# Kernel optimization log

Hardware: AMD Instinct MI355X
Metric: run time of the kernel (lower is better)

Reference implementation:

```python
import jax, jax.numpy as jnp
import numpy as np

N_NODES = 100000
N_EDGES = 3200000
EMBED = 64
DIMS = [(64, 32), (32, 16)]  # (in_dim, out_dim) per Aggregator layer
EPS = 1e-12


def setup_inputs() -> dict:
    key = jax.random.key(0)
    ks = jax.random.split(key, 16)
    inp = {
        "aux_info_all": jax.random.normal(ks[0], (N_NODES, 3), jnp.float32),
        "entity_embed": jax.random.normal(ks[1], (N_NODES, EMBED), jnp.float32) * 0.1,
        "aux_W": jax.random.normal(ks[2], (EMBED, 3), jnp.float32) * 0.3,
        "aux_b": jnp.zeros((EMBED,), jnp.float32),
        "edge_vals": jax.random.uniform(ks[3], (N_EDGES,), jnp.float32),
        "edge_rows": jax.random.randint(ks[4], (N_EDGES,), 0, N_NODES, jnp.int32),
        "edge_cols": jax.random.randint(ks[5], (N_EDGES,), 0, N_NODES, jnp.int32),
    }
    for li, (din, dout) in enumerate(DIMS):
        s = (2.0 / (din + dout)) ** 0.5  # xavier-ish scale
        inp[f"W1_{li}"] = jax.random.normal(ks[6 + 4 * li], (dout, din), jnp.float32) * s
        inp[f"b1_{li}"] = jnp.zeros((dout,), jnp.float32)
        inp[f"W2_{li}"] = jax.random.normal(ks[7 + 4 * li], (dout, din), jnp.float32) * s
        inp[f"b2_{li}"] = jnp.zeros((dout,), jnp.float32)
    return inp


def _l2norm(x):
    return x / jnp.maximum(jnp.linalg.norm(x, axis=1, keepdims=True), EPS)


def reference(aux_info_all, entity_embed, aux_W, aux_b,
              W1_0, b1_0, W2_0, b2_0, W1_1, b1_1, W2_1, b2_1,
              edge_vals, edge_rows, edge_cols):
    # holographic fusion: entity_embed * (1 + tanh(Linear(aux)))
    aux_vec = jnp.tanh(aux_info_all @ aux_W.T + aux_b)
    ego = entity_embed * (1.0 + aux_vec)  # [N, 64]
    all_embed = [ego]
    layers = [(W1_0, b1_0, W2_0, b2_0), (W1_1, b1_1, W2_1, b2_1)]
    for W1, b1, W2, b2 in layers:
        # sparse A_in @ ego: gather messages over edges, segment-sum by destination row
        msgs = edge_vals[:, None] * ego[edge_cols]  # [E, d]
        side = jax.ops.segment_sum(msgs, edge_rows, num_segments=N_NODES)  # [N, d]
        sum_e = jax.nn.leaky_relu((ego + side) @ W1.T + b1)  # bi-interaction branch 1
        bi_e = jax.nn.leaky_relu((ego * side) @ W2.T + b2)   # bi-interaction branch 2
        ego = sum_e + bi_e  # (dropout p=0 in eval)
        all_embed.append(_l2norm(ego))
    return jnp.concatenate(all_embed, axis=1)  # [N, 64+32+16]
```

## Files before the change

kernel.cpp:

```cpp
#include <hip/hip_runtime.h>
#include <math.h>

#define NN 100000
#define NE 3200000
#define OUTD 112
#define BROWS 512
#define NBUCK 196
#define FILL_CH 8192
#define FILL_B ((NE + FILL_CH - 1) / FILL_CH)
#define BLD1_T 1024
#define SORT_T 1024
#define FUSE_B ((NN * 64 + BLD1_T - 1) / BLD1_T)

__device__ inline unsigned short f32_to_bf16(float f) {
    unsigned u = __float_as_uint(f);
    u += 0x7FFFu + ((u >> 16) & 1u);
    return (unsigned short)(u >> 16);
}
__device__ inline float bf16_bits_to_f32(unsigned b) {
    return __uint_as_float(b << 16);
}

__global__ __launch_bounds__(BLD1_T) void prep_kernel(
    const int* __restrict__ rows,
    int* __restrict__ gcount,
    int* __restrict__ bhistT,
    const float* __restrict__ aux_info,
    const float* __restrict__ entity,
    const float* __restrict__ aux_W,
    const float* __restrict__ aux_b,
    unsigned short* __restrict__ ego0h,
    float* __restrict__ out)
{
    __shared__ int h[NBUCK];
    if (blockIdx.x < FILL_B) {
        for (int i = threadIdx.x; i < NBUCK; i += BLD1_T) h[i] = 0;
        __syncthreads();
        int base = blockIdx.x * FILL_CH;
        int nE = NE - base; if (nE > FILL_CH) nE = FILL_CH;
        for (int i = threadIdx.x; i < nE; i += BLD1_T)
            atomicAdd(&h[rows[base + i] >> 9], 1);
        __syncthreads();
        for (int i = threadIdx.x; i < NBUCK; i += BLD1_T) {
            int c = h[i];
            bhistT[i * FILL_B + blockIdx.x] = c;
            if (c) atomicAdd(&gcount[i], c);
        }
    } else {
        int idx = (blockIdx.x - FILL_B) * BLD1_T + threadIdx.x;
        if (idx >= NN * 64) return;
        int n = idx >> 6;
        int j = idx & 63;
        float a0 = aux_info[n * 3 + 0];
        float a1 = aux_info[n * 3 + 1];
        float a2 = aux_info[n * 3 + 2];
        float w0 = aux_W[j * 3 + 0];
        float w1 = aux_W[j * 3 + 1];
        float w2 = aux_W[j * 3 + 2];
        float t = tanhf(fmaf(a0, w0, fmaf(a1, w1, fmaf(a2, w2, aux_b[j]))));
        float e = entity[idx] * (1.0f + t);
        ego0h[idx] = f32_to_bf16(e);
        out[(size_t)n * OUTD + j] = e;
    }
}

__global__ void cursor_scan_kernel(const int* __restrict__ bhistT,
                                   const int* __restrict__ gcount,
                                   int* __restrict__ bucket_base,
                                   int* __restrict__ cursor) {
    static_assert(FILL_B <= 512, "scan width");
    __shared__ int sh[512];
    __shared__ int bb[256];
    int b = blockIdx.x;
    int t = threadIdx.x;
    int gv = (t < NBUCK) ? gcount[t] : 0;
    if (t < 256) bb[t] = gv;
    __syncthreads();
    for (int off = 1; off < 256; off <<= 1) {
        int u = (t >= off && t < 256) ? bb[t - off] : 0;
        __syncthreads();
        if (t < 256) bb[t] += u;
        __syncthreads();
    }
    int base_b = (b > 0) ? bb[b - 1] : 0;
    if (t == 0) bucket_base[b] = base_b;
    if (b == 0 && t == 0) bucket_base[NBUCK] = bb[NBUCK - 1];
    int v = (t < FILL_B) ? bhistT[b * FILL_B + t] : 0;
    sh[t] = v;
    __syncthreads();
    for (int off = 1; off < 512; off <<= 1) {
        int u = (t >= off) ? sh[t - off] : 0;
        __syncthreads();
        sh[t] += u;
        __syncthreads();
    }
    if (t < FILL_B) cursor[b * FILL_B + t] = base_b + sh[t] - v;
}

__global__ void bucket_fill_kernel(const int* __restrict__ rows,
                                   const int* __restrict__ cols,
                                   const float* __restrict__ vals,
                                   const int* __restrict__ cursor,
                                   int2* __restrict__ edges_b) {
    __shared__ int curs[NBUCK];
    int base = blockIdx.x * FILL_CH;
    int nE = NE - base; if (nE > FILL_CH) nE = FILL_CH;
    for (int i = threadIdx.x; i < NBUCK; i += BLD1_T)
        curs[i] = cursor[i * FILL_B + blockIdx.x];
    __syncthreads();
    for (int i = threadIdx.x; i < nE; i += BLD1_T) {
        int r = rows[base + i];
        int p = atomicAdd(&curs[r >> 9], 1);
        edges_b[p] = make_int2(cols[base + i] | ((r & (BROWS - 1)) << 17),
                               __float_as_int(vals[base + i]));
    }
}

__global__ __launch_bounds__(SORT_T) void csr_sort_kernel(
    const int2* __restrict__ edges_b,
    const int* __restrict__ bucket_base,
    unsigned int* __restrict__ edges,
    int* __restrict__ row_ptr) {
    __shared__ int cnt[BROWS];
    __shared__ int scn[BROWS];
    __shared__ int curs[BROWS];
    int b = blockIdx.x;
    int beg = bucket_base[b], end = bucket_base[b + 1];
    int t = threadIdx.x;
    if (t < BROWS) cnt[t] = 0;
    __syncthreads();
    for (int i = beg + t; i < end; i += SORT_T)
        atomicAdd(&cnt[(edges_b[i].x >> 17) & (BROWS - 1)], 1);
    __syncthreads();
    if (t < BROWS) scn[t] = cnt[t];
    __syncthreads();
    for (int off = 1; off < BROWS; off <<= 1) {
        int v = (t >= off && t < BROWS) ? scn[t - off] : 0;
        __syncthreads();
        if (t < BROWS) scn[t] += v;
        __syncthreads();
    }
    if (t < BROWS) {
        int excl = scn[t] - cnt[t];
        int n = b * BROWS + t;
        if (n <= NN) row_ptr[n] = beg + excl;
        curs[t] = beg + excl;
    }
    __syncthreads();
    for (int i = beg + t; i < end; i += SORT_T) {
        int2 e = edges_b[i];
        int rl = (e.x >> 17) & (BROWS - 1);
        int p = atomicAdd(&curs[rl], 1);
        unsigned int vb = f32_to_bf16(__int_as_float(e.y)) & 0x7FFFu;
        edges[p] = (unsigned int)(e.x & 0x1FFFF) | (vb << 17);
    }
}

template <int FO, int UU>
__device__ __forceinline__ void gacc(const uint4* __restrict__ egoh4,
                                     const unsigned int* __restrict__ edges,
                                     int i, int es, int fo, float a[8]) {
    constexpr int ES = 32 / FO;
    unsigned ew[UU];
    uint4 g[UU];
#pragma unroll
    for (int u = 0; u < UU; ++u) ew[u] = edges[i + u * ES + es];
#pragma unroll
    for (int u = 0; u < UU; ++u)
        g[u] = egoh4[(size_t)(ew[u] & 0x1FFFFu) * FO + fo];
#pragma unroll
    for (int u = 0; u < UU; ++u) {
        float v = __uint_as_float((ew[u] >> 1) & 0xFFFF0000u);
        a[0] = fmaf(v, __uint_as_float(g[u].x << 16), a[0]);
        a[1] = fmaf(v, __uint_as_float(g[u].x & 0xFFFF0000u), a[1]);
        a[2] = fmaf(v, __uint_as_float(g[u].y << 16), a[2]);
        a[3] = fmaf(v, __uint_as_float(g[u].y & 0xFFFF0000u), a[3]);
        a[4] = fmaf(v, __uint_as_float(g[u].z << 16), a[4]);
        a[5] = fmaf(v, __uint_as_float(g[u].z & 0xFFFF0000u), a[5]);
        a[6] = fmaf(v, __uint_as_float(g[u].w << 16), a[6]);
        a[7] = fmaf(v, __uint_as_float(g[u].w & 0xFFFF0000u), a[7]);
    }
}

template <int D>
__global__ __launch_bounds__(256) void gather_kernel(
    const uint4* __restrict__ egoh4,
    const unsigned int* __restrict__ edges,
    const int* __restrict__ row_ptr,
    float* __restrict__ side) {
    constexpr int FO = D / 8;
    constexpr int ES = 32 / FO;
    const int gt = blockIdx.x * 256 + threadIdx.x;
    const int n  = gt >> 5;
    const int li = gt & 31;
    const int es = li / FO;
    const int fo = li % FO;
    if (n >= NN) return;
    int beg = row_ptr[n];
    int end = row_ptr[n + 1];
    float a[8] = {0.f, 0.f, 0.f, 0.f, 0.f, 0.f, 0.f, 0.f};
    int i = beg;
    for (; i + 16 <= end; i += 16) gacc<FO, 16 / ES>(egoh4, edges, i, es, fo, a);
    for (; i + ES <= end; i += ES) gacc<FO, 1>(egoh4, edges, i, es, fo, a);
    if (i + es < end) {
        unsigned ew = edges[i + es];
        uint4 g = egoh4[(size_t)(ew & 0x1FFFFu) * FO + fo];
        float v = __uint_as_float((ew >> 1) & 0xFFFF0000u);
        a[0] = fmaf(v, __uint_as_float(g.x << 16), a[0]);
        a[1] = fmaf(v, __uint_as_float(g.x & 0xFFFF0000u), a[1]);
        a[2] = fmaf(v, __uint_as_float(g.y << 16), a[2]);
        a[3] = fmaf(v, __uint_as_float(g.y & 0xFFFF0000u), a[3]);
        a[4] = fmaf(v, __uint_as_float(g.z << 16), a[4]);
        a[5] = fmaf(v, __uint_as_float(g.z & 0xFFFF0000u), a[5]);
        a[6] = fmaf(v, __uint_as_float(g.w << 16), a[6]);
        a[7] = fmaf(v, __uint_as_float(g.w & 0xFFFF0000u), a[7]);
    }
#pragma unroll
    for (int st = FO; st < 32; st <<= 1) {
#pragma unroll
        for (int q = 0; q < 8; ++q) a[q] += __shfl_xor(a[q], st);
    }
    if (es == 0)
        *(float4*)&side[(size_t)n * D + fo * 8] =
            make_float4(a[0], a[1], a[2], a[3]);
    else if (es == 1)
        *(float4*)&side[(size_t)n * D + fo * 8 + 4] =
            make_float4(a[4], a[5], a[6], a[7]);
}

template <int DIN, int DOUT, int NB>
__global__ __launch_bounds__(256, 4) void layer_kernel(
    const float* __restrict__ ego, int ego_stride,
    const float* __restrict__ side,
    const float* __restrict__ W1, const float* __restrict__ b1,
    const float* __restrict__ W2, const float* __restrict__ b2,
    float* __restrict__ ego_next,
    unsigned short* __restrict__ ego_next_h,
    float* __restrict__ out, int out_off)
{
    constexpr int RW  = DIN + 4;
    constexpr int CH  = DIN / 4;
    constexpr int NPT = NB * DOUT / 256;
    static_assert(NB * DOUT % 256 == 0, "");
    static_assert(NPT == 4, "register budget tuned for NPT=4");

    __shared__ float sArr[NB][RW];
    __shared__ float pArr[NB][RW];
    __shared__ float4 W1q[CH * DOUT];
    __shared__ float4 W2q[CH * DOUT];

    const int node0 = blockIdx.x * NB;

    for (int t = threadIdx.x; t < CH * DOUT; t += 256) {
        int j  = t / CH;
        int kg = t - j * CH;
        W1q[kg * DOUT + j] = *(const float4*)&W1[j * DIN + kg * 4];
        W2q[kg * DOUT + j] = *(const float4*)&W2[j * DIN + kg * 4];
    }

    for (int i = threadIdx.x; i < NB * CH; i += 256) {
        int m = i / CH;
        int c = i - m * CH;
        int n = node0 + m;
        if (n < NN) {
            float4 e  = *(const float4*)&ego[(size_t)n * ego_stride + c * 4];
            float4 sd = *(const float4*)&side[(size_t)n * DIN + c * 4];
            *(float4*)&sArr[m][c * 4] =
                make_float4(e.x + sd.x, e.y + sd.y, e.z + sd.z, e.w + sd.w);
            *(float4*)&pArr[m][c * 4] =
                make_float4(e.x * sd.x, e.y * sd.y, e.z * sd.z, e.w * sd.w);
        }
    }
    __syncthreads();

    const int j     = threadIdx.x % DOUT;
    const int slot  = threadIdx.x / DOUT;
    const int mbase = slot * NPT;

    float acc1[NPT], acc2[NPT];
    {
        float bb1 = b1[j], bb2 = b2[j];
#pragma unroll
        for (int m8 = 0; m8 < NPT; ++m8) { acc1[m8] = bb1; acc2[m8] = bb2; }
    }

#pragma unroll 2
    for (int kg = 0; kg < CH; ++kg) {
        float4 w1 = W1q[kg * DOUT + j];
        float4 w2 = W2q[kg * DOUT + j];
#pragma unroll
        for (int m8 = 0; m8 < NPT; ++m8) {
            float4 sv = *(const float4*)&sArr[mbase + m8][kg * 4];
            float4 pv = *(const float4*)&pArr[mbase + m8][kg * 4];
            acc1[m8] = fmaf(sv.x, w1.x, acc1[m8]);
            acc1[m8] = fmaf(sv.y, w1.y, acc1[m8]);
            acc1[m8] = fmaf(sv.z, w1.z, acc1[m8]);
            acc1[m8] = fmaf(sv.w, w1.w, acc1[m8]);
            acc2[m8] = fmaf(pv.x, w2.x, acc2[m8]);
            acc2[m8] = fmaf(pv.y, w2.y, acc2[m8]);
            acc2[m8] = fmaf(pv.z, w2.z, acc2[m8]);
            acc2[m8] = fmaf(pv.w, w2.w, acc2[m8]);
        }
    }

#pragma unroll
    for (int m8 = 0; m8 < NPT; ++m8) {
        int n = node0 + mbase + m8;
        float s  = acc1[m8]; s  = (s  > 0.0f) ? s  : 0.01f * s;
        float bb = acc2[m8]; bb = (bb > 0.0f) ? bb : 0.01f * bb;
        float v = s + bb;
        float sq = v * v;
#pragma unroll
        for (int off = DOUT / 2; off > 0; off >>= 1)
            sq += __shfl_xor(sq, off, DOUT);
        float norm = sqrtf(sq);
        norm = (norm > 1e-12f) ? norm : 1e-12f;
        if (n < NN) {
            if (ego_next)   ego_next[(size_t)n * DOUT + j] = v;
            if (ego_next_h) ego_next_h[(size_t)n * DOUT + j] = f32_to_bf16(v);
            out[(size_t)n * OUTD + out_off + j] = v / norm;
        }
    }
}

extern "C" void kernel_launch(void* const* d_in, const int* in_sizes, int n_in,
                              void* d_out, int out_size, void* d_ws, size_t ws_size,
                              hipStream_t stream) {
    const float* aux_info  = (const float*)d_in[0];
    const float* entity    = (const float*)d_in[1];
    const float* aux_W     = (const float*)d_in[2];
    const float* aux_b     = (const float*)d_in[3];
    const float* edge_vals = (const float*)d_in[4];
    const int*   edge_rows = (const int*)d_in[5];
    const int*   edge_cols = (const int*)d_in[6];
    const float* W1_0 = (const float*)d_in[7];
    const float* b1_0 = (const float*)d_in[8];
    const float* W2_0 = (const float*)d_in[9];
    const float* b2_0 = (const float*)d_in[10];
    const float* W1_1 = (const float*)d_in[11];
    const float* b1_1 = (const float*)d_in[12];
    const float* W2_1 = (const float*)d_in[13];
    const float* b2_1 = (const float*)d_in[14];
    float* out = (float*)d_out;

    float* region0 = (float*)d_ws;
    int2*  edges_b = (int2*)region0;
    float* side0   = region0;
    unsigned short* ego0h = (unsigned short*)(region0 + (size_t)NE * 2);
    unsigned short* ego1h = ego0h;
    unsigned int* edges = (unsigned int*)((float*)ego0h + (size_t)NN * 32);
    float* ego1  = (float*)(edges + NE);
    float* side1 = ego1 + (size_t)NN * 32;
    int* row_ptr     = (int*)(side1 + (size_t)NN * 32);
    int* bucket_base = row_ptr + NN + 1;
    int* gcount      = bucket_base + NBUCK + 1;
    int* bhistT      = gcount + NBUCK;
    int* cursor      = bhistT + (size_t)NBUCK * FILL_B;

    hipMemsetAsync(gcount, 0, (size_t)NBUCK * sizeof(int), stream);
    prep_kernel<<<FILL_B + FUSE_B, BLD1_T, 0, stream>>>(
        edge_rows, gcount, bhistT, aux_info, entity, aux_W, aux_b, ego0h, out);
    cursor_scan_kernel<<<NBUCK, 512, 0, stream>>>(bhistT, gcount, bucket_base, cursor);
    bucket_fill_kernel<<<FILL_B, BLD1_T, 0, stream>>>(
        edge_rows, edge_cols, edge_vals, cursor, edges_b);
    csr_sort_kernel<<<NBUCK, SORT_T, 0, stream>>>(edges_b, bucket_base, edges, row_ptr);

    gather_kernel<64><<<NN / 8, 256, 0, stream>>>(
        (const uint4*)ego0h, edges, row_ptr, side0);
    layer_kernel<64, 32, 32><<<(NN + 31) / 32, 256, 0, stream>>>(
        out, OUTD, side0, W1_0, b1_0, W2_0, b2_0, ego1, ego1h, out, 64);
    gather_kernel<32><<<NN / 8, 256, 0, stream>>>(
        (const uint4*)ego1h, edges, row_ptr, side1);
    layer_kernel<32, 16, 64><<<(NN + 63) / 64, 256, 0, stream>>>(
        ego1, 32, side1, W1_1, b1_1, W2_1, b2_1, nullptr, nullptr, out, 96);
}
```

Before: 379.7 us.

## Move per-row counting into bucket fill, split key/value buffers, vectorize prep

```diff
diff --git a/kernel.cpp b/kernel.cpp
--- a/kernel.cpp
+++ b/kernel.cpp
@@ -10,7 +10,7 @@
 #define FILL_B ((NE + FILL_CH - 1) / FILL_CH)
 #define BLD1_T 1024
 #define SORT_T 1024
-#define FUSE_B ((NN * 64 + BLD1_T - 1) / BLD1_T)
+#define FUSE_B ((NN * 16 + BLD1_T - 1) / BLD1_T)
 
 __device__ inline unsigned short f32_to_bf16(float f) {
     unsigned u = __float_as_uint(f);
@@ -48,19 +48,29 @@
         }
     } else {
         int idx = (blockIdx.x - FILL_B) * BLD1_T + threadIdx.x;
-        if (idx >= NN * 64) return;
-        int n = idx >> 6;
-        int j = idx & 63;
+        if (idx >= NN * 16) return;
+        int n  = idx >> 4;
+        int j0 = (idx & 15) * 4;
         float a0 = aux_info[n * 3 + 0];
         float a1 = aux_info[n * 3 + 1];
         float a2 = aux_info[n * 3 + 2];
-        float w0 = aux_W[j * 3 + 0];
-        float w1 = aux_W[j * 3 + 1];
-        float w2 = aux_W[j * 3 + 2];
-        float t = tanhf(fmaf(a0, w0, fmaf(a1, w1, fmaf(a2, w2, aux_b[j]))));
-        float e = entity[idx] * (1.0f + t);
-        ego0h[idx] = f32_to_bf16(e);
-        out[(size_t)n * OUTD + j] = e;
+        float4 w0 = *(const float4*)&aux_W[j0 * 3 + 0];
+        float4 w1 = *(const float4*)&aux_W[j0 * 3 + 4];
+        float4 w2 = *(const float4*)&aux_W[j0 * 3 + 8];
+        float4 bq = *(const float4*)&aux_b[j0];
+        float4 ev = *(const float4*)&entity[(size_t)n * 64 + j0];
+        float4 r;
+        r.x = ev.x * (1.0f + tanhf(fmaf(a0, w0.x, fmaf(a1, w0.y, fmaf(a2, w0.z, bq.x)))));
+        r.y = ev.y * (1.0f + tanhf(fmaf(a0, w0.w, fmaf(a1, w1.x, fmaf(a2, w1.y, bq.y)))));
+        r.z = ev.z * (1.0f + tanhf(fmaf(a0, w1.z, fmaf(a1, w1.w, fmaf(a2, w2.x, bq.z)))));
+        r.w = ev.w * (1.0f + tanhf(fmaf(a0, w2.y, fmaf(a1, w2.z, fmaf(a2, w2.w, bq.w)))));
+        ushort4 hq;
+        hq.x = f32_to_bf16(r.x);
+        hq.y = f32_to_bf16(r.y);
+        hq.z = f32_to_bf16(r.z);
+        hq.w = f32_to_bf16(r.w);
+        *(ushort4*)&ego0h[(size_t)n * 64 + j0] = hq;
+        *(float4*)&out[(size_t)n * OUTD + j0] = r;
     }
 }
 
@@ -101,7 +111,9 @@
                                    const int* __restrict__ cols,
                                    const float* __restrict__ vals,
                                    const int* __restrict__ cursor,
-                                   int2* __restrict__ edges_b) {
+                                   int* __restrict__ rcount,
+                                   unsigned int* __restrict__ bkeys,
+                                   float* __restrict__ bvals) {
     __shared__ int curs[NBUCK];
     int base = blockIdx.x * FILL_CH;
     int nE = NE - base; if (nE > FILL_CH) nE = FILL_CH;
@@ -110,49 +122,56 @@
     __syncthreads();
     for (int i = threadIdx.x; i < nE; i += BLD1_T) {
         int r = rows[base + i];
+        int c = __builtin_nontemporal_load(&cols[base + i]);
+        float v = __builtin_nontemporal_load(&vals[base + i]);
         int p = atomicAdd(&curs[r >> 9], 1);
-        edges_b[p] = make_int2(cols[base + i] | ((r & (BROWS - 1)) << 17),
-                               __float_as_int(vals[base + i]));
-    }
+        bkeys[p] = (unsigned int)c | ((r & (BROWS - 1)) << 17);
+        bvals[p] = v;
+        atomicAdd(&rcount[r], 1);
+    }
+}
+
+__global__ void row_scan_kernel(const int* __restrict__ rcount,
+                                const int* __restrict__ bucket_base,
+                                int* __restrict__ row_ptr) {
+    __shared__ int sc[BROWS];
+    int b = blockIdx.x;
+    int t = threadIdx.x;
+    int n = b * BROWS + t;
+    int c = (n < NN) ? rcount[n] : 0;
+    sc[t] = c;
+    __syncthreads();
+    for (int off = 1; off < BROWS; off <<= 1) {
+        int u = (t >= off) ? sc[t - off] : 0;
+        __syncthreads();
+        sc[t] += u;
+        __syncthreads();
+    }
+    if (n <= NN) row_ptr[n] = bucket_base[b] + sc[t] - c;
 }
 
 __global__ __launch_bounds__(SORT_T) void csr_sort_kernel(
-    const int2* __restrict__ edges_b,
+    const unsigned int* __restrict__ bkeys,
+    const float* __restrict__ bvals,
     const int* __restrict__ bucket_base,
-    unsigned int* __restrict__ edges,
-    int* __restrict__ row_ptr) {
-    __shared__ int cnt[BROWS];
-    __shared__ int scn[BROWS];
+    const int* __restrict__ row_ptr,
+    unsigned int* __restrict__ edges) {
     __shared__ int curs[BROWS];
     int b = blockIdx.x;
     int beg = bucket_base[b], end = bucket_base[b + 1];
     int t = threadIdx.x;
-    if (t < BROWS) cnt[t] = 0;
-    __syncthreads();
-    for (int i = beg + t; i < end; i += SORT_T)
-        atomicAdd(&cnt[(edges_b[i].x >> 17) & (BROWS - 1)], 1);
-    __syncthreads();
-    if (t < BROWS) scn[t] = cnt[t];
-    __syncthreads();
-    for (int off = 1; off < BROWS; off <<= 1) {
-        int v = (t >= off && t < BROWS) ? scn[t - off] : 0;
-        __syncthreads();
-        if (t < BROWS) scn[t] += v;
-        __syncthreads();
-    }
     if (t < BROWS) {
-        int excl = scn[t] - cnt[t];
         int n = b * BROWS + t;
-        if (n <= NN) row_ptr[n] = beg + excl;
-        curs[t] = beg + excl;
+        curs[t] = (n < NN) ? row_ptr[n] : 0;
     }
     __syncthreads();
     for (int i = beg + t; i < end; i += SORT_T) {
-        int2 e = edges_b[i];
-        int rl = (e.x >> 17) & (BROWS - 1);
+        unsigned int k = __builtin_nontemporal_load(&bkeys[i]);
+        float v = __builtin_nontemporal_load(&bvals[i]);
+        int rl = (k >> 17) & (BROWS - 1);
         int p = atomicAdd(&curs[rl], 1);
-        unsigned int vb = f32_to_bf16(__int_as_float(e.y)) & 0x7FFFu;
-        edges[p] = (unsigned int)(e.x & 0x1FFFF) | (vb << 17);
+        unsigned int vb = f32_to_bf16(v) & 0x7FFFu;
+        edges[p] = (k & 0x1FFFF) | (vb << 17);
     }
 }
 
@@ -164,7 +183,8 @@
     unsigned ew[UU];
     uint4 g[UU];
 #pragma unroll
-    for (int u = 0; u < UU; ++u) ew[u] = edges[i + u * ES + es];
+    for (int u = 0; u < UU; ++u)
+        ew[u] = __builtin_nontemporal_load(&edges[i + u * ES + es]);
 #pragma unroll
     for (int u = 0; u < UU; ++u)
         g[u] = egoh4[(size_t)(ew[u] & 0x1FFFFu) * FO + fo];
@@ -203,7 +223,7 @@
     for (; i + 16 <= end; i += 16) gacc<FO, 16 / ES>(egoh4, edges, i, es, fo, a);
     for (; i + ES <= end; i += ES) gacc<FO, 1>(egoh4, edges, i, es, fo, a);
     if (i + es < end) {
-        unsigned ew = edges[i + es];
+        unsigned ew = __builtin_nontemporal_load(&edges[i + es]);
         uint4 g = egoh4[(size_t)(ew & 0x1FFFFu) * FO + fo];
         float v = __uint_as_float((ew >> 1) & 0xFFFF0000u);
         a[0] = fmaf(v, __uint_as_float(g.x << 16), a[0]);
@@ -344,8 +364,9 @@
     float* out = (float*)d_out;
 
     float* region0 = (float*)d_ws;
-    int2*  edges_b = (int2*)region0;
-    float* side0   = region0;
+    unsigned int* bkeys = (unsigned int*)region0;
+    float* bvals = region0 + NE;
+    float* side0 = region0;
     unsigned short* ego0h = (unsigned short*)(region0 + (size_t)NE * 2);
     unsigned short* ego1h = ego0h;
     unsigned int* edges = (unsigned int*)((float*)ego0h + (size_t)NN * 32);
@@ -354,16 +375,19 @@
     int* row_ptr     = (int*)(side1 + (size_t)NN * 32);
     int* bucket_base = row_ptr + NN + 1;
     int* gcount      = bucket_base + NBUCK + 1;
-    int* bhistT      = gcount + NBUCK;
+    int* rcount      = gcount + NBUCK;
+    int* bhistT      = rcount + NN;
     int* cursor      = bhistT + (size_t)NBUCK * FILL_B;
 
-    hipMemsetAsync(gcount, 0, (size_t)NBUCK * sizeof(int), stream);
+    hipMemsetAsync(gcount, 0, (size_t)(NBUCK + NN) * sizeof(int), stream);
     prep_kernel<<<FILL_B + FUSE_B, BLD1_T, 0, stream>>>(
         edge_rows, gcount, bhistT, aux_info, entity, aux_W, aux_b, ego0h, out);
     cursor_scan_kernel<<<NBUCK, 512, 0, stream>>>(bhistT, gcount, bucket_base, cursor);
     bucket_fill_kernel<<<FILL_B, BLD1_T, 0, stream>>>(
-        edge_rows, edge_cols, edge_vals, cursor, edges_b);
-    csr_sort_kernel<<<NBUCK, SORT_T, 0, stream>>>(edges_b, bucket_base, edges, row_ptr);
+        edge_rows, edge_cols, edge_vals, cursor, rcount, bkeys, bvals);
+    row_scan_kernel<<<NBUCK, BROWS, 0, stream>>>(rcount, bucket_base, row_ptr);
+    csr_sort_kernel<<<NBUCK, SORT_T, 0, stream>>>(
+        bkeys, bvals, bucket_base, row_ptr, edges);
 
     gather_kernel<64><<<NN / 8, 256, 0, stream>>>(
         (const uint4*)ego0h, edges, row_ptr, side0);
```

Result: slower. 501.9 us (+32.2%).
